# Performance work log

Hardware: AMD Instinct MI355X
Metric: run time of the kernel (lower is better)

Reference implementation:

```python
import jax, jax.numpy as jnp
import numpy as np

B, S, D = 4, 2048, 1024
EPS = 1e-5

def setup_inputs() -> dict:
    key = jax.random.key(0)
    ks = jax.random.split(key, 6)
    return {
        "x": jax.random.normal(ks[0], (B, S, D), dtype=jnp.float32),
        "ln_w": jax.random.uniform(ks[1], (D,), dtype=jnp.float32),
        "wq": jax.random.normal(ks[2], (D, D), dtype=jnp.float32) * (1.0 / np.sqrt(D)),
        "wk": jax.random.normal(ks[3], (D, D), dtype=jnp.float32) * (1.0 / np.sqrt(D)),
        "wv": jax.random.normal(ks[4], (D, D), dtype=jnp.float32) * (1.0 / np.sqrt(D)),
        "wo": jax.random.normal(ks[5], (D, D), dtype=jnp.float32) * (1.0 / np.sqrt(D)),
    }

def reference(x, ln_w, wq, wk, wv, wo):
    # LayerNorm (bias=False): normalize over last dim, scale by ln_w
    mu = jnp.mean(x, axis=-1, keepdims=True)
    var = jnp.mean(jnp.square(x - mu), axis=-1, keepdims=True)
    h = (x - mu) * jax.lax.rsqrt(var + EPS) * ln_w
    # QKV projections (torch Linear: y = h @ W.T)
    q = jnp.einsum("bsd,ed->bse", h, wq)
    k = jnp.einsum("bsd,ed->bse", h, wk)
    v = jnp.einsum("bsd,ed->bse", h, wv)
    # Attention: NOTE source has no 1/sqrt(d) scaling
    scores = jnp.einsum("bqd,bkd->bqk", q, k)
    attn = jax.nn.softmax(scores, axis=-1)
    ctx = jnp.einsum("bqk,bkd->bqd", attn, v)
    return jnp.einsum("bsd,ed->bse", ctx, wo)
```

## Files before the change

kernel.cpp:

```cpp
#include <hip/hip_runtime.h>
#include <hip/hip_bf16.h>

using bf16 = __hip_bfloat16;
typedef __attribute__((ext_vector_type(8))) short short8;
typedef __attribute__((ext_vector_type(4))) float f32x4;
typedef __attribute__((ext_vector_type(4))) unsigned short us4;

static constexpr int Bn = 4, Sn = 2048, Dn = 1024;
static constexpr int ROWS = Bn * Sn;
static constexpr float EPS = 1e-5f;

__device__ __forceinline__ void splitf(float v, bf16& hi, bf16& lo) {
    hi = __float2bfloat16(v);
    lo = __float2bfloat16(v - __bfloat162float(hi));
}

__device__ __forceinline__ void gload_lds16(const void* g, void* l) {
    __builtin_amdgcn_global_load_lds(
        (__attribute__((address_space(1))) void*)(void*)g,
        (__attribute__((address_space(3))) void*)l, 16, 0, 0);
}

__global__ __launch_bounds__(256) void wsplit3_kernel(const float* __restrict__ w,
                                                      bf16* __restrict__ out) {
    const int i = blockIdx.x * 256 + threadIdx.x;
    const float4 v = reinterpret_cast<const float4*>(w)[i];
    const int row = i >> 8, c = (i & 255) << 2;
    alignas(8) bf16 h[4], l[4];
    splitf(v.x, h[0], l[0]); splitf(v.y, h[1], l[1]);
    splitf(v.z, h[2], l[2]); splitf(v.w, h[3], l[3]);
    bf16* o = out + (size_t)row * 3072 + c;
    *reinterpret_cast<us4*>(o)        = *reinterpret_cast<const us4*>(h);
    *reinterpret_cast<us4*>(o + 1024) = *reinterpret_cast<const us4*>(h);
    *reinterpret_cast<us4*>(o + 2048) = *reinterpret_cast<const us4*>(l);
}

__global__ __launch_bounds__(256) void wsplit_hi_kernel(const float* __restrict__ w,
                                                        bf16* __restrict__ hi) {
    const int i = blockIdx.x * 256 + threadIdx.x;
    const float4 v = reinterpret_cast<const float4*>(w)[i];
    alignas(8) bf16 h[4];
    bf16 l;
    splitf(v.x, h[0], l); splitf(v.y, h[1], l);
    splitf(v.z, h[2], l); splitf(v.w, h[3], l);
    *reinterpret_cast<us4*>(hi + i * 4) = *reinterpret_cast<const us4*>(h);
}

__global__ __launch_bounds__(256) void ln3_kernel(const float* __restrict__ x,
                                                  const float* __restrict__ w,
                                                  bf16* __restrict__ h3) {
    const int row = blockIdx.x, tid = threadIdx.x;
    const int lane = tid & 63, wave = tid >> 6;
    const float4 v = reinterpret_cast<const float4*>(x + (size_t)row * Dn)[tid];
    float s  = v.x + v.y + v.z + v.w;
    float s2 = v.x*v.x + v.y*v.y + v.z*v.z + v.w*v.w;
    #pragma unroll
    for (int off = 32; off > 0; off >>= 1) {
        s  += __shfl_down(s,  off, 64);
        s2 += __shfl_down(s2, off, 64);
    }
    __shared__ float red[8];
    if (lane == 0) { red[wave] = s; red[4 + wave] = s2; }
    __syncthreads();
    s  = red[0] + red[1] + red[2] + red[3];
    s2 = red[4] + red[5] + red[6] + red[7];
    const float mu  = s * (1.0f / Dn);
    const float var = s2 * (1.0f / Dn) - mu * mu;
    const float rs  = rsqrtf(var + EPS);
    const float4 wv = reinterpret_cast<const float4*>(w)[tid];
    alignas(8) bf16 h[4], l[4];
    splitf((v.x - mu) * rs * wv.x, h[0], l[0]);
    splitf((v.y - mu) * rs * wv.y, h[1], l[1]);
    splitf((v.z - mu) * rs * wv.z, h[2], l[2]);
    splitf((v.w - mu) * rs * wv.w, h[3], l[3]);
    bf16* o = h3 + (size_t)row * 3072 + tid * 4;
    *reinterpret_cast<us4*>(o)        = *reinterpret_cast<const us4*>(h);
    *reinterpret_cast<us4*>(o + 1024) = *reinterpret_cast<const us4*>(l);
    *reinterpret_cast<us4*>(o + 2048) = *reinterpret_cast<const us4*>(h);
}

__global__ __launch_bounds__(256) void softmax_kernel(float* __restrict__ scores) {
    const int row = blockIdx.x, tid = threadIdx.x;
    const int lane = tid & 63, wave = tid >> 6;
    float* r = scores + (size_t)row * Sn;
    const float4 v0 = reinterpret_cast<const float4*>(r)[tid];
    const float4 v1 = reinterpret_cast<const float4*>(r)[tid + 256];
    float m = fmaxf(fmaxf(fmaxf(v0.x, v0.y), fmaxf(v0.z, v0.w)),
                    fmaxf(fmaxf(v1.x, v1.y), fmaxf(v1.z, v1.w)));
    #pragma unroll
    for (int off = 32; off > 0; off >>= 1) m = fmaxf(m, __shfl_down(m, off, 64));
    __shared__ float red[8];
    if (lane == 0) red[wave] = m;
    __syncthreads();
    m = fmaxf(fmaxf(red[0], red[1]), fmaxf(red[2], red[3]));
    float e[8];
    e[0] = expf(v0.x - m); e[1] = expf(v0.y - m);
    e[2] = expf(v0.z - m); e[3] = expf(v0.w - m);
    e[4] = expf(v1.x - m); e[5] = expf(v1.y - m);
    e[6] = expf(v1.z - m); e[7] = expf(v1.w - m);
    float s = e[0]+e[1]+e[2]+e[3]+e[4]+e[5]+e[6]+e[7];
    #pragma unroll
    for (int off = 32; off > 0; off >>= 1) s += __shfl_down(s, off, 64);
    if (lane == 0) red[4 + wave] = s;
    __syncthreads();
    s = red[4] + red[5] + red[6] + red[7];
    const float inv = 1.0f / s;
    bf16* hi = reinterpret_cast<bf16*>(r);
    #pragma unroll
    for (int j = 0; j < 4; ++j) hi[tid*4 + j]        = __float2bfloat16(e[j] * inv);
    #pragma unroll
    for (int j = 0; j < 4; ++j) hi[1024 + tid*4 + j] = __float2bfloat16(e[4+j] * inv);
}

template <int SM>
__global__ __launch_bounds__(256)
void gemm3(const bf16* __restrict__ A, int lda, long long sA,
           const bf16* __restrict__ B, int ldb, long long sB,
           float* __restrict__ Cf, bf16* __restrict__ Cb,
           int ldc, long long sC, int K) {
    const int tid = threadIdx.x;
    const int lane = tid & 63, wave = tid >> 6;
    const int bm = blockIdx.x, bn = blockIdx.y;
    const long long aBase = (long long)blockIdx.z * sA;
    const long long bBase = (long long)blockIdx.z * sB;
    const long long cBase = (long long)blockIdx.z * sC;

    __shared__ bf16 sAh[128*32];
    __shared__ bf16 sBh[128*32];

    f32x4 acc[4][4];
    #pragma unroll
    for (int i = 0; i < 4; ++i)
        #pragma unroll
        for (int j = 0; j < 4; ++j) acc[i][j] = f32x4{0.f, 0.f, 0.f, 0.f};

    const int wm = wave >> 1, wn = wave & 1;
    const int fr = lane & 15;
    const int kb = (lane >> 4) * 8;

    for (int k0 = 0; k0 < K; k0 += 32) {
        #pragma unroll
        for (int i = 0; i < 2; ++i) {
            const int idx = (i * 4 + wave) * 64 + lane;
            const int row = idx >> 2;
            const int seg = (idx & 3) * 8;
            const int lds_off = (i * 4 + wave) * 512;
            gload_lds16(A + aBase + (long long)(bm * 128 + row) * lda + k0 + seg, sAh + lds_off);
            gload_lds16(B + bBase + (long long)(bn * 128 + row) * ldb + k0 + seg, sBh + lds_off);
        }
        __syncthreads();
        short8 ah[4], bh[4];
        #pragma unroll
        for (int t = 0; t < 4; ++t) {
            ah[t] = *reinterpret_cast<const short8*>(sAh + (wm*64 + t*16 + fr) * 32 + kb);
            bh[t] = *reinterpret_cast<const short8*>(sBh + (wn*64 + t*16 + fr) * 32 + kb);
        }
        #pragma unroll
        for (int mi = 0; mi < 4; ++mi)
            #pragma unroll
            for (int ni = 0; ni < 4; ++ni)
                acc[mi][ni] = __builtin_amdgcn_mfma_f32_16x16x32_bf16(ah[mi], bh[ni], acc[mi][ni], 0, 0, 0);
        __syncthreads();
    }

    #pragma unroll
    for (int mi = 0; mi < 4; ++mi) {
        const int row0 = bm * 128 + wm * 64 + mi * 16 + (lane >> 4) * 4;
        #pragma unroll
        for (int ni = 0; ni < 4; ++ni) {
            const int col = bn * 128 + wn * 64 + ni * 16 + fr;
            if constexpr (SM == 0) {
                #pragma unroll
                for (int r = 0; r < 4; ++r)
                    Cf[cBase + (long long)(row0 + r) * ldc + col] = acc[mi][ni][r];
            } else if constexpr (SM == 2) {
                alignas(8) bf16 th[4];
                #pragma unroll
                for (int r = 0; r < 4; ++r) th[r] = __float2bfloat16(acc[mi][ni][r]);
                const long long o = cBase + (long long)col * ldc + row0;
                *reinterpret_cast<us4*>(Cb + o) = *reinterpret_cast<const us4*>(th);
            } else {
                #pragma unroll
                for (int r = 0; r < 4; ++r)
                    Cb[cBase + (long long)(row0 + r) * ldc + col] = __float2bfloat16(acc[mi][ni][r]);
            }
        }
    }
}

template <int SM>
__global__ __launch_bounds__(512, 2)
void gemm8(const bf16* __restrict__ A, int lda, long long sA,
           const bf16* __restrict__ B, int ldb, long long sB,
           float* __restrict__ Cf, bf16* __restrict__ Cq, bf16* __restrict__ Ck,
           int ldc, long long sC, int K) {
    const int tid = threadIdx.x;
    const int lane = tid & 63, wave = tid >> 6;
    const int wm = wave >> 2, wn = wave & 3;
    const int fl = lane & 15, s0 = lane >> 4;
    const int bm = blockIdx.x, bn = blockIdx.y;

    __shared__ bf16 lds[3 * 16384];

    const int tr = tid >> 2;
    const int sg = (tid & 3) ^ ((tr >> 1) & 3);
    const bf16* gA = A + (long long)blockIdx.z * sA + (long long)(bm*256 + tr) * lda + sg*8;
    const bf16* gB = B + (long long)blockIdx.z * sB + (long long)(bn*256 + tr) * ldb + sg*8;
    bf16* ldsw = lds + wave * 512;
    const long long a128 = (long long)128 * lda, b128 = (long long)128 * ldb;

    const int sw = (s0 ^ ((fl >> 1) & 3)) * 8;
    const int aoff = (wm*128 + fl) * 32 + sw;
    const int boff = 8192 + (wn*64 + fl) * 32 + sw;

    f32x4 acc[8][4];
    #pragma unroll
    for (int i = 0; i < 8; ++i)
        #pragma unroll
        for (int j = 0; j < 4; ++j) acc[i][j] = f32x4{0.f, 0.f, 0.f, 0.f};

    const int NT = K >> 5;
    gload_lds16(gA,             ldsw);
    gload_lds16(gA + a128,      ldsw + 4096);
    gload_lds16(gB,             ldsw + 8192);
    gload_lds16(gB + b128,      ldsw + 12288);
    gload_lds16(gA + 32,        ldsw + 16384);
    gload_lds16(gA + a128 + 32, ldsw + 16384 + 4096);
    gload_lds16(gB + 32,        ldsw + 16384 + 8192);
    gload_lds16(gB + b128 + 32, ldsw + 16384 + 12288);
    asm volatile("s_waitcnt vmcnt(4)" ::: "memory");
    __builtin_amdgcn_s_barrier();

    int c0 = 0;
    for (int kt = 0; kt < NT; ++kt) {
        const int c2 = (c0 >= 1) ? c0 - 1 : 2;
        int ktp = kt + 2; if (ktp >= NT) ktp = 0;
        const int kp = ktp << 5;
        const bf16* ab = lds + c0 * 16384;
        bf16* pw = ldsw + c2 * 16384;

        gload_lds16(gA + kp,        pw);
        gload_lds16(gA + kp + a128, pw + 4096);
        short8 bfr[4], afr[4];
        #pragma unroll
        for (int ni = 0; ni < 4; ++ni) bfr[ni] = *reinterpret_cast<const short8*>(ab + boff + ni*512);
        #pragma unroll
        for (int mi = 0; mi < 4; ++mi) afr[mi] = *reinterpret_cast<const short8*>(ab + aoff + mi*512);
        __builtin_amdgcn_s_barrier();
        __builtin_amdgcn_s_setprio(1);
        #pragma unroll
        for (int mi = 0; mi < 4; ++mi)
            #pragma unroll
            for (int ni = 0; ni < 4; ++ni)
                acc[mi][ni] = __builtin_amdgcn_mfma_f32_16x16x32_bf16(afr[mi], bfr[ni], acc[mi][ni], 0, 0, 0);
        __builtin_amdgcn_s_setprio(0);
        __builtin_amdgcn_s_barrier();

        gload_lds16(gB + kp,        pw + 8192);
        gload_lds16(gB + kp + b128, pw + 12288);
        short8 af2[4];
        #pragma unroll
        for (int mi = 0; mi < 4; ++mi) af2[mi] = *reinterpret_cast<const short8*>(ab + aoff + (mi+4)*512);
        __builtin_amdgcn_s_barrier();
        __builtin_amdgcn_s_setprio(1);
        #pragma unroll
        for (int mi = 0; mi < 4; ++mi)
            #pragma unroll
            for (int ni = 0; ni < 4; ++ni)
                acc[mi+4][ni] = __builtin_amdgcn_mfma_f32_16x16x32_bf16(af2[mi], bfr[ni], acc[mi+4][ni], 0, 0, 0);
        __builtin_amdgcn_s_setprio(0);
        asm volatile("s_waitcnt vmcnt(4)" ::: "memory");
        __builtin_amdgcn_s_barrier();
        c0 = (c0 < 2) ? c0 + 1 : 0;
    }

    const long long cB = (long long)blockIdx.z * sC;
    #pragma unroll
    for (int mi = 0; mi < 8; ++mi) {
        const int row0 = bm*256 + wm*128 + mi*16 + s0*4;
        #pragma unroll
        for (int ni = 0; ni < 4; ++ni) {
            const int col = bn*256 + wn*64 + ni*16 + fl;
            if constexpr (SM == 0) {
                #pragma unroll
                for (int r = 0; r < 4; ++r)
                    Cf[cB + (long long)(row0 + r) * ldc + col] = acc[mi][ni][r];
            } else if constexpr (SM == 4) {
                #pragma unroll
                for (int r = 0; r < 4; ++r) {
                    const long long o = cB + (long long)(row0 + r) * ldc + col;
                    Cf[o] += acc[mi][ni][r];
                }
            } else {
                if (col < 1024) {
                    #pragma unroll
                    for (int r = 0; r < 4; ++r) {
                        bf16 h, l; splitf(acc[mi][ni][r], h, l);
                        const long long o = (long long)(row0 + r) * ldc + col;
                        Cq[o] = l; Cq[o + 1024] = h;
                    }
                } else {
                    const int c = col - 1024;
                    #pragma unroll
                    for (int r = 0; r < 4; ++r) {
                        bf16 h, l; splitf(acc[mi][ni][r], h, l);
                        const long long o = (long long)(row0 + r) * ldc + c;
                        Ck[o] = h; Ck[o + 1024] = l;
                    }
                }
            }
        }
    }
}

extern "C" void kernel_launch(void* const* d_in, const int* in_sizes, int n_in,
                              void* d_out, int out_size, void* d_ws, size_t ws_size,
                              hipStream_t stream) {
    const float* x    = (const float*)d_in[0];
    const float* ln_w = (const float*)d_in[1];
    const float* wq   = (const float*)d_in[2];
    const float* wk   = (const float*)d_in[3];
    const float* wv   = (const float*)d_in[4];
    const float* wo   = (const float*)d_in[5];
    float* out = (float*)d_out;

    const size_t M1 = 1u << 20;
    bf16* base = (bf16*)d_ws;
    bf16* h3    = base;
    bf16* wqk3  = base + 24*M1;
    bf16* wv_hi = base + 30*M1;
    float* scores = (float*)base;
    bf16* q2    = base + 32*M1;
    bf16* k2    = base + 48*M1;
    bf16* vt    = base + 64*M1;
    bf16* ctx   = base + 32*M1;
    bf16* wo_hi = base + 40*M1;

    wsplit3_kernel<<<dim3(1024), 256, 0, stream>>>(wq, wqk3);
    wsplit3_kernel<<<dim3(1024), 256, 0, stream>>>(wk, wqk3 + (size_t)1024 * 3072);
    wsplit_hi_kernel<<<dim3(1024), 256, 0, stream>>>(wv, wv_hi);

    ln3_kernel<<<ROWS, 256, 0, stream>>>(x, ln_w, h3);

    gemm8<1><<<dim3(ROWS/256, 2*Dn/256), 512, 0, stream>>>(
        h3, 3072, 0, wqk3, 3072, 0,
        nullptr, q2, k2, 2048, 0, 3072);

    gemm3<2><<<dim3(Sn/128, Dn/128, Bn), 256, 0, stream>>>(
        h3, 3072, (long long)Sn * 3072, wv_hi, 1024, 0,
        nullptr, vt, Sn, (long long)Dn * Sn, 1024);

    gemm8<0><<<dim3(Sn/256, Sn/256, Bn), 512, 0, stream>>>(
        q2, 2048, (long long)Sn * 2048, k2, 2048, (long long)Sn * 2048,
        scores, nullptr, nullptr, Sn, (long long)Sn * Sn, 2048);
    gemm8<4><<<dim3(Sn/256, Sn/256, Bn), 512, 0, stream>>>(
        q2 + 1024, 2048, (long long)Sn * 2048, k2, 2048, (long long)Sn * 2048,
        scores, nullptr, nullptr, Sn, (long long)Sn * Sn, 1024);

    softmax_kernel<<<ROWS, 256, 0, stream>>>(scores);

    wsplit_hi_kernel<<<dim3(1024), 256, 0, stream>>>(wo, wo_hi);

    gemm3<3><<<dim3(Sn/128, Dn/128, Bn), 256, 0, stream>>>(
        (const bf16*)scores, 2*Sn, (long long)Sn * 2*Sn,
        vt, Sn, (long long)Dn * Sn,
        nullptr, ctx, Dn, (long long)Sn * Dn, Sn);

    gemm3<0><<<dim3(ROWS/128, Dn/128), 256, 0, stream>>>(
        ctx, Dn, 0, wo_hi, Dn, 0,
        out, nullptr, Dn, 0, Dn);
}
```

Measured before the change: 465.7 us.

## Fuse split-bf16 GEMM passes via chunk remapping and deeper LDS pipelining

Replaces the triplicated hi/lo operand layouts (K=3072) with compact hi|lo layouts (K=2048) and a new gemm256 kernel. It reads the hi or lo chunk of each operand through RA/RB bitmasks, so the three split products (hi*hi, hi*lo, lo*hi) come from one 48-step K loop. This removes the redundant third copy written by the weight-split and layernorm kernels, and merges the two score GEMM launches (including the read-modify-write accumulate pass) into one. The main loop is rewritten as an 8-phase macro with a 4-slot LDS pipeline (128 KB) and interleaved prefetch. The larger LDS footprint may limit occupancy.

```diff
diff --git a/kernel.cpp b/kernel.cpp
--- a/kernel.cpp
+++ b/kernel.cpp
@@ -21,7 +21,7 @@
         (__attribute__((address_space(3))) void*)l, 16, 0, 0);
 }
 
-__global__ __launch_bounds__(256) void wsplit3_kernel(const float* __restrict__ w,
+__global__ __launch_bounds__(256) void wsplit2_kernel(const float* __restrict__ w,
                                                       bf16* __restrict__ out) {
     const int i = blockIdx.x * 256 + threadIdx.x;
     const float4 v = reinterpret_cast<const float4*>(w)[i];
@@ -29,10 +29,9 @@
     alignas(8) bf16 h[4], l[4];
     splitf(v.x, h[0], l[0]); splitf(v.y, h[1], l[1]);
     splitf(v.z, h[2], l[2]); splitf(v.w, h[3], l[3]);
-    bf16* o = out + (size_t)row * 3072 + c;
+    bf16* o = out + (size_t)row * 2048 + c;
     *reinterpret_cast<us4*>(o)        = *reinterpret_cast<const us4*>(h);
-    *reinterpret_cast<us4*>(o + 1024) = *reinterpret_cast<const us4*>(h);
-    *reinterpret_cast<us4*>(o + 2048) = *reinterpret_cast<const us4*>(l);
+    *reinterpret_cast<us4*>(o + 1024) = *reinterpret_cast<const us4*>(l);
 }
 
 __global__ __launch_bounds__(256) void wsplit_hi_kernel(const float* __restrict__ w,
@@ -46,9 +45,9 @@
     *reinterpret_cast<us4*>(hi + i * 4) = *reinterpret_cast<const us4*>(h);
 }
 
-__global__ __launch_bounds__(256) void ln3_kernel(const float* __restrict__ x,
+__global__ __launch_bounds__(256) void ln2_kernel(const float* __restrict__ x,
                                                   const float* __restrict__ w,
-                                                  bf16* __restrict__ h3) {
+                                                  bf16* __restrict__ h2) {
     const int row = blockIdx.x, tid = threadIdx.x;
     const int lane = tid & 63, wave = tid >> 6;
     const float4 v = reinterpret_cast<const float4*>(x + (size_t)row * Dn)[tid];
@@ -73,10 +72,9 @@
     splitf((v.y - mu) * rs * wv.y, h[1], l[1]);
     splitf((v.z - mu) * rs * wv.z, h[2], l[2]);
     splitf((v.w - mu) * rs * wv.w, h[3], l[3]);
-    bf16* o = h3 + (size_t)row * 3072 + tid * 4;
+    bf16* o = h2 + (size_t)row * 2048 + tid * 4;
     *reinterpret_cast<us4*>(o)        = *reinterpret_cast<const us4*>(h);
     *reinterpret_cast<us4*>(o + 1024) = *reinterpret_cast<const us4*>(l);
-    *reinterpret_cast<us4*>(o + 2048) = *reinterpret_cast<const us4*>(h);
 }
 
 __global__ __launch_bounds__(256) void softmax_kernel(float* __restrict__ scores) {
@@ -188,125 +186,126 @@
     }
 }
 
-template <int SM>
+#define G256_PHASE(BUF, KS, MG, READB, ST_T, ST_MAT, ST_KS, VM)                              \
+    {                                                                                        \
+        const int slotA_ = (((BUF) * 2 + 0) * 2 + (KS)) * 8192;                              \
+        const int slotB_ = (((BUF) * 2 + 1) * 2 + (KS)) * 8192;                              \
+        if (READB) {                                                                         \
+            _Pragma("unroll")                                                                \
+            for (int n = 0; n < 4; ++n)                                                      \
+                bfr[n] = *reinterpret_cast<const short8*>(lds + slotB_ + boff + n * 512);    \
+        }                                                                                    \
+        short8 afr[4];                                                                       \
+        _Pragma("unroll")                                                                    \
+        for (int m = 0; m < 4; ++m)                                                          \
+            afr[m] = *reinterpret_cast<const short8*>(lds + slotA_ + aoff + ((MG)*4 + m) * 512); \
+        {                                           \
+            const int tc_ = ((ST_T) < 47) ? (ST_T) : 47;                                     \
+            const int slot_ = ((((ST_T) & 1) * 2 + (ST_MAT)) * 2 + (ST_KS)) * 8192;          \
+            const int R_ = (ST_MAT) ? RB : RA;                                               \
+            const int kb_ = (((R_ >> (tc_ >> 4)) & 1) << 10) + ((tc_ & 15) << 6) + ((ST_KS) << 5); \
+            const bf16* g_ = (ST_MAT) ? gB : gA;                                             \
+            const int ld_ = (ST_MAT) ? ldb : lda;                                            \
+            gload_lds16(g_ + (long long)srow * ld_ + kb_ + schunk, lds + slot_ + wave * 512);\
+            gload_lds16(g_ + (long long)(128 + srow) * ld_ + kb_ + schunk,                   \
+                        lds + slot_ + 4096 + wave * 512);                                    \
+        }                                                                                    \
+        __builtin_amdgcn_s_barrier();                                                        \
+        asm volatile("s_waitcnt lgkmcnt(0)" ::: "memory");                                   \
+        __builtin_amdgcn_sched_barrier(0);                                                   \
+        __builtin_amdgcn_s_setprio(1);                                                       \
+        _Pragma("unroll")                                                                    \
+        for (int m = 0; m < 4; ++m)                                                          \
+            _Pragma("unroll")                                                                \
+            for (int n = 0; n < 4; ++n)                                                      \
+                acc[(MG)*4 + m][n] = __builtin_amdgcn_mfma_f32_16x16x32_bf16(                \
+                    afr[m], bfr[n], acc[(MG)*4 + m][n], 0, 0, 0);                            \
+        __builtin_amdgcn_s_setprio(0);                                                       \
+        if (VM) asm volatile("s_waitcnt vmcnt(4)" ::: "memory");                             \
+        __builtin_amdgcn_s_barrier();                                                        \
+    }
+
+template <int RA, int RB, int SM>
 __global__ __launch_bounds__(512, 2)
-void gemm8(const bf16* __restrict__ A, int lda, long long sA,
-           const bf16* __restrict__ B, int ldb, long long sB,
-           float* __restrict__ Cf, bf16* __restrict__ Cq, bf16* __restrict__ Ck,
-           int ldc, long long sC, int K) {
+void gemm256(const bf16* __restrict__ A, int lda, long long sA,
+             const bf16* __restrict__ B, int ldb, long long sB,
+             float* __restrict__ Cf, bf16* __restrict__ Cq, bf16* __restrict__ Ck,
+             int ldc, long long sC) {
     const int tid = threadIdx.x;
     const int lane = tid & 63, wave = tid >> 6;
     const int wm = wave >> 2, wn = wave & 3;
-    const int fl = lane & 15, s0 = lane >> 4;
+    const int fr = lane & 15, s0 = lane >> 4;
     const int bm = blockIdx.x, bn = blockIdx.y;
 
-    __shared__ bf16 lds[3 * 16384];
-
-    const int tr = tid >> 2;
-    const int sg = (tid & 3) ^ ((tr >> 1) & 3);
-    const bf16* gA = A + (long long)blockIdx.z * sA + (long long)(bm*256 + tr) * lda + sg*8;
-    const bf16* gB = B + (long long)blockIdx.z * sB + (long long)(bn*256 + tr) * ldb + sg*8;
-    bf16* ldsw = lds + wave * 512;
-    const long long a128 = (long long)128 * lda, b128 = (long long)128 * ldb;
-
-    const int sw = (s0 ^ ((fl >> 1) & 3)) * 8;
-    const int aoff = (wm*128 + fl) * 32 + sw;
-    const int boff = 8192 + (wn*64 + fl) * 32 + sw;
+    __shared__ bf16 lds[8 * 8192];
+
+    const bf16* gA = A + (long long)blockIdx.z * sA + (long long)(bm * 256) * lda;
+    const bf16* gB = B + (long long)blockIdx.z * sB + (long long)(bn * 256) * ldb;
+
+    const int srow = tid >> 2;
+    const int schunk = (((tid & 3) ^ ((tid >> 3) & 3))) * 8;
+
+    const int rsw = (s0 ^ ((fr >> 1) & 3)) * 8;
+    const int aoff = (wm * 128 + fr) * 32 + rsw;
+    const int boff = (wn * 64 + fr) * 32 + rsw;
 
     f32x4 acc[8][4];
     #pragma unroll
     for (int i = 0; i < 8; ++i)
         #pragma unroll
         for (int j = 0; j < 4; ++j) acc[i][j] = f32x4{0.f, 0.f, 0.f, 0.f};
-
-    const int NT = K >> 5;
-    gload_lds16(gA,             ldsw);
-    gload_lds16(gA + a128,      ldsw + 4096);
-    gload_lds16(gB,             ldsw + 8192);
-    gload_lds16(gB + b128,      ldsw + 12288);
-    gload_lds16(gA + 32,        ldsw + 16384);
-    gload_lds16(gA + a128 + 32, ldsw + 16384 + 4096);
-    gload_lds16(gB + 32,        ldsw + 16384 + 8192);
-    gload_lds16(gB + b128 + 32, ldsw + 16384 + 12288);
-    asm volatile("s_waitcnt vmcnt(4)" ::: "memory");
-    __builtin_amdgcn_s_barrier();
-
-    int c0 = 0;
-    for (int kt = 0; kt < NT; ++kt) {
-        const int c2 = (c0 >= 1) ? c0 - 1 : 2;
-        int ktp = kt + 2; if (ktp >= NT) ktp = 0;
-        const int kp = ktp << 5;
-        const bf16* ab = lds + c0 * 16384;
-        bf16* pw = ldsw + c2 * 16384;
-
-        gload_lds16(gA + kp,        pw);
-        gload_lds16(gA + kp + a128, pw + 4096);
-        short8 bfr[4], afr[4];
-        #pragma unroll
-        for (int ni = 0; ni < 4; ++ni) bfr[ni] = *reinterpret_cast<const short8*>(ab + boff + ni*512);
-        #pragma unroll
-        for (int mi = 0; mi < 4; ++mi) afr[mi] = *reinterpret_cast<const short8*>(ab + aoff + mi*512);
-        __builtin_amdgcn_s_barrier();
-        __builtin_amdgcn_s_setprio(1);
-        #pragma unroll
-        for (int mi = 0; mi < 4; ++mi)
-            #pragma unroll
-            for (int ni = 0; ni < 4; ++ni)
-                acc[mi][ni] = __builtin_amdgcn_mfma_f32_16x16x32_bf16(afr[mi], bfr[ni], acc[mi][ni], 0, 0, 0);
-        __builtin_amdgcn_s_setprio(0);
-        __builtin_amdgcn_s_barrier();
-
-        gload_lds16(gB + kp,        pw + 8192);
-        gload_lds16(gB + kp + b128, pw + 12288);
-        short8 af2[4];
-        #pragma unroll
-        for (int mi = 0; mi < 4; ++mi) af2[mi] = *reinterpret_cast<const short8*>(ab + aoff + (mi+4)*512);
-        __builtin_amdgcn_s_barrier();
-        __builtin_amdgcn_s_setprio(1);
-        #pragma unroll
-        for (int mi = 0; mi < 4; ++mi)
-            #pragma unroll
-            for (int ni = 0; ni < 4; ++ni)
-                acc[mi+4][ni] = __builtin_amdgcn_mfma_f32_16x16x32_bf16(af2[mi], bfr[ni], acc[mi+4][ni], 0, 0, 0);
-        __builtin_amdgcn_s_setprio(0);
+    short8 bfr[4];
+
+    {
+        #pragma unroll
+        for (int st = 0; st < 6; ++st) {
+            const int t_ = (st < 4) ? 0 : 1;
+            const int mat_ = st & 1;
+            const int ks_ = (st < 4) ? (st >> 1) : 0;
+            const int slot_ = (((t_ & 1) * 2 + mat_) * 2 + ks_) * 8192;
+            const int R_ = mat_ ? RB : RA;
+            const int kb_ = (((R_ >> (t_ >> 4)) & 1) << 10) + ((t_ & 15) << 6) + (ks_ << 5);
+            const bf16* g_ = mat_ ? gB : gA;
+            const int ld_ = mat_ ? ldb : lda;
+            gload_lds16(g_ + (long long)srow * ld_ + kb_ + schunk, lds + slot_ + wave * 512);
+            gload_lds16(g_ + (long long)(128 + srow) * ld_ + kb_ + schunk,
+                        lds + slot_ + 4096 + wave * 512);
+        }
         asm volatile("s_waitcnt vmcnt(4)" ::: "memory");
         __builtin_amdgcn_s_barrier();
-        c0 = (c0 < 2) ? c0 + 1 : 0;
+    }
+
+    for (int j = 0; j < 24; ++j) {
+        const int t0 = 2 * j, t1 = 2 * j + 1;
+        G256_PHASE(0, 0, 0, true,  t1,     0, 1, false)
+        G256_PHASE(0, 0, 1, false, t1,     1, 1, false)
+        G256_PHASE(0, 1, 0, true,  t0 + 2, 0, 0, false)
+        G256_PHASE(0, 1, 1, false, t0 + 2, 1, 0, true)
+        G256_PHASE(1, 0, 0, true,  t0 + 2, 0, 1, false)
+        G256_PHASE(1, 0, 1, false, t0 + 2, 1, 1, false)
+        G256_PHASE(1, 1, 0, true,  t1 + 2, 0, 0, false)
+        G256_PHASE(1, 1, 1, false, t1 + 2, 1, 0, true)
     }
 
     const long long cB = (long long)blockIdx.z * sC;
     #pragma unroll
     for (int mi = 0; mi < 8; ++mi) {
-        const int row0 = bm*256 + wm*128 + mi*16 + s0*4;
+        const int row0 = bm * 256 + wm * 128 + mi * 16 + s0 * 4;
         #pragma unroll
         for (int ni = 0; ni < 4; ++ni) {
-            const int col = bn*256 + wn*64 + ni*16 + fl;
+            const int col = bn * 256 + wn * 64 + ni * 16 + fr;
             if constexpr (SM == 0) {
                 #pragma unroll
                 for (int r = 0; r < 4; ++r)
                     Cf[cB + (long long)(row0 + r) * ldc + col] = acc[mi][ni][r];
-            } else if constexpr (SM == 4) {
+            } else {
                 #pragma unroll
                 for (int r = 0; r < 4; ++r) {
-                    const long long o = cB + (long long)(row0 + r) * ldc + col;
-                    Cf[o] += acc[mi][ni][r];
-                }
-            } else {
-                if (col < 1024) {
-                    #pragma unroll
-                    for (int r = 0; r < 4; ++r) {
-                        bf16 h, l; splitf(acc[mi][ni][r], h, l);
-                        const long long o = (long long)(row0 + r) * ldc + col;
-                        Cq[o] = l; Cq[o + 1024] = h;
-                    }
-                } else {
-                    const int c = col - 1024;
-                    #pragma unroll
-                    for (int r = 0; r < 4; ++r) {
-                        bf16 h, l; splitf(acc[mi][ni][r], h, l);
-                        const long long o = (long long)(row0 + r) * ldc + c;
-                        Ck[o] = h; Ck[o + 1024] = l;
-                    }
+                    bf16 h, l; splitf(acc[mi][ni][r], h, l);
+                    bf16* dst = (col < 1024) ? Cq : Ck;
+                    const int c = col & 1023;
+                    const long long o = (long long)(row0 + r) * 2048 + c;
+                    dst[o] = h; dst[o + 1024] = l;
                 }
             }
         }
@@ -326,36 +325,33 @@
 
     const size_t M1 = 1u << 20;
     bf16* base = (bf16*)d_ws;
-    bf16* h3    = base;
-    bf16* wqk3  = base + 24*M1;
-    bf16* wv_hi = base + 30*M1;
+    bf16* h2    = base;
+    bf16* w2    = base + 16*M1;
+    bf16* wv_hi = base + 20*M1;
     float* scores = (float*)base;
     bf16* q2    = base + 32*M1;
     bf16* k2    = base + 48*M1;
     bf16* vt    = base + 64*M1;
-    bf16* ctx   = base + 32*M1;
-    bf16* wo_hi = base + 40*M1;
-
-    wsplit3_kernel<<<dim3(1024), 256, 0, stream>>>(wq, wqk3);
-    wsplit3_kernel<<<dim3(1024), 256, 0, stream>>>(wk, wqk3 + (size_t)1024 * 3072);
+    bf16* ctx   = base + 72*M1;
+    bf16* wo_hi = base + 80*M1;
+
+    wsplit2_kernel<<<dim3(1024), 256, 0, stream>>>(wq, w2);
+    wsplit2_kernel<<<dim3(1024), 256, 0, stream>>>(wk, w2 + (size_t)1024 * 2048);
     wsplit_hi_kernel<<<dim3(1024), 256, 0, stream>>>(wv, wv_hi);
 
-    ln3_kernel<<<ROWS, 256, 0, stream>>>(x, ln_w, h3);
-
-    gemm8<1><<<dim3(ROWS/256, 2*Dn/256), 512, 0, stream>>>(
-        h3, 3072, 0, wqk3, 3072, 0,
-        nullptr, q2, k2, 2048, 0, 3072);
+    ln2_kernel<<<ROWS, 256, 0, stream>>>(x, ln_w, h2);
+
+    gemm256<0b010, 0b100, 1><<<dim3(ROWS/256, 2*Dn/256), 512, 0, stream>>>(
+        h2, 2048, 0, w2, 2048, 0,
+        nullptr, q2, k2, 0, 0);
 
     gemm3<2><<<dim3(Sn/128, Dn/128, Bn), 256, 0, stream>>>(
-        h3, 3072, (long long)Sn * 3072, wv_hi, 1024, 0,
+        h2, 2048, (long long)Sn * 2048, wv_hi, 1024, 0,
         nullptr, vt, Sn, (long long)Dn * Sn, 1024);
 
-    gemm8<0><<<dim3(Sn/256, Sn/256, Bn), 512, 0, stream>>>(
+    gemm256<0b100, 0b010, 0><<<dim3(Sn/256, Sn/256, Bn), 512, 0, stream>>>(
         q2, 2048, (long long)Sn * 2048, k2, 2048, (long long)Sn * 2048,
-        scores, nullptr, nullptr, Sn, (long long)Sn * Sn, 2048);
-    gemm8<4><<<dim3(Sn/256, Sn/256, Bn), 512, 0, stream>>>(
-        q2 + 1024, 2048, (long long)Sn * 2048, k2, 2048, (long long)Sn * 2048,
-        scores, nullptr, nullptr, Sn, (long long)Sn * Sn, 1024);
+        scores, nullptr, nullptr, Sn, (long long)Sn * Sn);
 
     softmax_kernel<<<ROWS, 256, 0, stream>>>(scores);
 
```

Measured after the change: 436.5 us. 6.3% less time.
